# Kernel tuning notes

Hardware: AMD Instinct MI355X
Metric: run time of the kernel (lower is better)

The kernel has to match this reference:

```python
import jax, jax.numpy as jnp
import numpy as np

HIDDEN = 1024
SEQ = 32768


def setup_inputs() -> dict:
    key = jax.random.key(0)
    k1, k2, k3, k4 = jax.random.split(key, 4)
    scale = 1.0 / np.sqrt(HIDDEN)
    return {
        "hidden": jax.random.normal(k1, (HIDDEN,), dtype=jnp.float32),
        "encoder_outputs": jax.random.normal(k2, (SEQ, HIDDEN), dtype=jnp.float32),
        "W": jax.random.normal(k3, (HIDDEN, HIDDEN), dtype=jnp.float32) * scale,
        "b": jax.random.normal(k4, (HIDDEN,), dtype=jnp.float32) * scale,
    }


def reference(hidden, encoder_outputs, W, b):
    # method == 'general': energy_i = Linear(enc_i); score_i = hidden . energy_i
    # Batched: energies = (enc @ W.T + b) @ hidden   -> [S]
    proj = jnp.einsum("sh,oh->so", encoder_outputs, W) + b  # [S, H]
    energies = proj @ hidden                                  # [S]
    attn = jax.nn.softmax(energies, axis=-1)                  # softmax over seq
    return attn[None, None, :]                                # [1, 1, S]
```

## Files before the change

### kernel.cpp

```cpp
#include <hip/hip_runtime.h>
#include <math.h>

#define H 1024
#define S 32768

__global__ void matvec_v_kernel(const float* __restrict__ W,
                                const float* __restrict__ hidden,
                                float* __restrict__ v) {
    __shared__ float sh[H];
    __shared__ float4 red[256];
    const int t = threadIdx.x;
    const int b = blockIdx.x;
    const int c = t & 7;
    const int j = t >> 3;

    *reinterpret_cast<float4*>(&sh[t * 4]) =
        *reinterpret_cast<const float4*>(&hidden[t * 4]);
    __syncthreads();

    const int colbase = b * 32 + c * 4;
    float4 acc = make_float4(0.f, 0.f, 0.f, 0.f);
#pragma unroll 8
    for (int k = 0; k < 32; ++k) {
        const int o = j + 32 * k;
        const float hv = sh[o];
        const float4 w = *reinterpret_cast<const float4*>(&W[(size_t)o * H + colbase]);
        acc.x += hv * w.x; acc.y += hv * w.y;
        acc.z += hv * w.z; acc.w += hv * w.w;
    }
    red[t] = acc;
    __syncthreads();
#pragma unroll
    for (int off = 128; off >= 8; off >>= 1) {
        if (t < off) {
            float4 a = red[t], bb = red[t + off];
            a.x += bb.x; a.y += bb.y; a.z += bb.z; a.w += bb.w;
            red[t] = a;
        }
        __syncthreads();
    }
    if (t < 8)
        *reinterpret_cast<float4*>(&v[b * 32 + t * 4]) = red[t];
}

__global__ void energies_kernel(const float* __restrict__ enc,
                                const float* __restrict__ v,
                                float* __restrict__ energies,
                                float* __restrict__ mpart,
                                float* __restrict__ spart) {
    const int wave = threadIdx.x >> 6;
    const int lane = threadIdx.x & 63;
    const int gwave = blockIdx.x * 4 + wave;
    const int s0 = gwave * 4;

    float4 vv[4];
#pragma unroll
    for (int j = 0; j < 4; ++j)
        vv[j] = *reinterpret_cast<const float4*>(&v[j * 256 + lane * 4]);

    float4 ev[4][4];
#pragma unroll
    for (int r = 0; r < 4; ++r) {
        const float* row = enc + (size_t)(s0 + r) * H;
#pragma unroll
        for (int j = 0; j < 4; ++j)
            ev[r][j] = *reinterpret_cast<const float4*>(&row[j * 256 + lane * 4]);
    }

    float e[4];
#pragma unroll
    for (int r = 0; r < 4; ++r) {
        float acc = ev[r][0].x * vv[0].x + ev[r][0].y * vv[0].y +
                    ev[r][0].z * vv[0].z + ev[r][0].w * vv[0].w;
#pragma unroll
        for (int j = 1; j < 4; ++j) {
            acc += ev[r][j].x * vv[j].x + ev[r][j].y * vv[j].y +
                   ev[r][j].z * vv[j].z + ev[r][j].w * vv[j].w;
        }
#pragma unroll
        for (int off = 32; off > 0; off >>= 1)
            acc += __shfl_xor(acc, off, 64);
        e[r] = acc;
    }

    if (lane == 0) {
        energies[s0 + 0] = e[0];
        energies[s0 + 1] = e[1];
        energies[s0 + 2] = e[2];
        energies[s0 + 3] = e[3];
    }

    const float mw = fmaxf(fmaxf(e[0], e[1]), fmaxf(e[2], e[3]));
    const float sw = __expf(e[0] - mw) + __expf(e[1] - mw) +
                     __expf(e[2] - mw) + __expf(e[3] - mw);

    __shared__ float lm[4], ls[4];
    if (lane == 0) { lm[wave] = mw; ls[wave] = sw; }
    __syncthreads();
    if (threadIdx.x == 0) {
        const float m = fmaxf(fmaxf(lm[0], lm[1]), fmaxf(lm[2], lm[3]));
        const float s = ls[0] * __expf(lm[0] - m) + ls[1] * __expf(lm[1] - m) +
                        ls[2] * __expf(lm[2] - m) + ls[3] * __expf(lm[3] - m);
        mpart[blockIdx.x] = m;
        spart[blockIdx.x] = s;
    }
}

__global__ void finalize_kernel(const float* __restrict__ energies,
                                const float* __restrict__ mpart,
                                const float* __restrict__ spart,
                                float* __restrict__ out) {
    const int t = threadIdx.x;
    const int lane = t & 63;
    const int wave = t >> 6;
    __shared__ float rm[4], rs[4];

    const float4 ma = *reinterpret_cast<const float4*>(&mpart[t * 8]);
    const float4 mb = *reinterpret_cast<const float4*>(&mpart[t * 8 + 4]);
    const float4 sa = *reinterpret_cast<const float4*>(&spart[t * 8]);
    const float4 sb = *reinterpret_cast<const float4*>(&spart[t * 8 + 4]);

    float mt = fmaxf(fmaxf(fmaxf(ma.x, ma.y), fmaxf(ma.z, ma.w)),
                     fmaxf(fmaxf(mb.x, mb.y), fmaxf(mb.z, mb.w)));
#pragma unroll
    for (int off = 32; off > 0; off >>= 1)
        mt = fmaxf(mt, __shfl_xor(mt, off, 64));
    if (lane == 0) rm[wave] = mt;
    __syncthreads();
    const float gm = fmaxf(fmaxf(rm[0], rm[1]), fmaxf(rm[2], rm[3]));

    float st = sa.x * __expf(ma.x - gm) + sa.y * __expf(ma.y - gm) +
               sa.z * __expf(ma.z - gm) + sa.w * __expf(ma.w - gm) +
               sb.x * __expf(mb.x - gm) + sb.y * __expf(mb.y - gm) +
               sb.z * __expf(mb.z - gm) + sb.w * __expf(mb.w - gm);
#pragma unroll
    for (int off = 32; off > 0; off >>= 1)
        st += __shfl_xor(st, off, 64);
    if (lane == 0) rs[wave] = st;
    __syncthreads();
    const float inv = 1.0f / (rs[0] + rs[1] + rs[2] + rs[3]);

    const int i = blockIdx.x * 256 + t;
    out[i] = __expf(energies[i] - gm) * inv;
}

extern "C" void kernel_launch(void* const* d_in, const int* in_sizes, int n_in,
                              void* d_out, int out_size, void* d_ws, size_t ws_size,
                              hipStream_t stream) {
    const float* hidden = (const float*)d_in[0];
    const float* enc    = (const float*)d_in[1];
    const float* W      = (const float*)d_in[2];
    float* out = (float*)d_out;

    float* v        = (float*)d_ws;
    float* energies = v + H;
    float* mpart    = energies + S;
    float* spart    = mpart + 2048;

    matvec_v_kernel<<<32, 256, 0, stream>>>(W, hidden, v);
    energies_kernel<<<2048, 256, 0, stream>>>(enc, v, energies, mpart, spart);
    finalize_kernel<<<128, 256, 0, stream>>>(energies, mpart, spart, out);
}
```

Baseline: 206.6 us.

## Split matvec across more blocks and map 16-lane groups per row in energies kernel

The W·hidden matvec now runs on 64 blocks of 16 columns each instead of 32 blocks of 32 columns, to spread the W read over more CUs. The energies kernel stages v in shared memory and gives each row to a 16-lane group that loads its row in two batches of 8 float4. This needs only a 4-step shuffle reduction per row and cuts register pressure from 16 float4 of encoder data to 8. The block still covers 16 rows, but memory access per lane is now strided in 256-byte chunks per row, which may change coalescing behaviour.

```diff
diff --git a/kernel.cpp b/kernel.cpp
--- a/kernel.cpp
+++ b/kernel.cpp
@@ -11,18 +11,18 @@
     __shared__ float4 red[256];
     const int t = threadIdx.x;
     const int b = blockIdx.x;
-    const int c = t & 7;
-    const int j = t >> 3;
+    const int c = t & 3;
+    const int j = t >> 2;
 
     *reinterpret_cast<float4*>(&sh[t * 4]) =
         *reinterpret_cast<const float4*>(&hidden[t * 4]);
     __syncthreads();
 
-    const int colbase = b * 32 + c * 4;
+    const int colbase = b * 16 + c * 4;
     float4 acc = make_float4(0.f, 0.f, 0.f, 0.f);
-#pragma unroll 8
-    for (int k = 0; k < 32; ++k) {
-        const int o = j + 32 * k;
+#pragma unroll
+    for (int k = 0; k < 16; ++k) {
+        const int o = j + 64 * k;
         const float hv = sh[o];
         const float4 w = *reinterpret_cast<const float4*>(&W[(size_t)o * H + colbase]);
         acc.x += hv * w.x; acc.y += hv * w.y;
@@ -31,7 +31,7 @@
     red[t] = acc;
     __syncthreads();
 #pragma unroll
-    for (int off = 128; off >= 8; off >>= 1) {
+    for (int off = 128; off >= 4; off >>= 1) {
         if (t < off) {
             float4 a = red[t], bb = red[t + off];
             a.x += bb.x; a.y += bb.y; a.z += bb.z; a.w += bb.w;
@@ -39,8 +39,8 @@
         }
         __syncthreads();
     }
-    if (t < 8)
-        *reinterpret_cast<float4*>(&v[b * 32 + t * 4]) = red[t];
+    if (t < 4)
+        *reinterpret_cast<float4*>(&v[b * 16 + t * 4]) = red[t];
 }
 
 __global__ void energies_kernel(const float* __restrict__ enc,
@@ -48,56 +48,56 @@
                                 float* __restrict__ energies,
                                 float* __restrict__ mpart,
                                 float* __restrict__ spart) {
-    const int wave = threadIdx.x >> 6;
-    const int lane = threadIdx.x & 63;
-    const int gwave = blockIdx.x * 4 + wave;
-    const int s0 = gwave * 4;
+    __shared__ float sv[H];
+    __shared__ float lm[4], ls[4];
+    const int t = threadIdx.x;
+    const int wave = t >> 6;
+    const int lane = t & 63;
+    const int grp  = lane >> 4;
+    const int gl   = lane & 15;
 
-    float4 vv[4];
+    *reinterpret_cast<float4*>(&sv[t * 4]) =
+        *reinterpret_cast<const float4*>(&v[t * 4]);
+
+    const int row = blockIdx.x * 16 + wave * 4 + grp;
+    const float* rp = enc + (size_t)row * H + gl * 4;
+    __syncthreads();
+
+    float4 ev[8];
+    float acc = 0.f;
+
 #pragma unroll
-    for (int j = 0; j < 4; ++j)
-        vv[j] = *reinterpret_cast<const float4*>(&v[j * 256 + lane * 4]);
-
-    float4 ev[4][4];
+    for (int s = 0; s < 8; ++s)
+        ev[s] = *reinterpret_cast<const float4*>(&rp[s * 64]);
 #pragma unroll
-    for (int r = 0; r < 4; ++r) {
-        const float* row = enc + (size_t)(s0 + r) * H;
+    for (int s = 0; s < 8; ++s) {
+        const float4 vv = *reinterpret_cast<const float4*>(&sv[s * 64 + gl * 4]);
+        acc += ev[s].x * vv.x + ev[s].y * vv.y + ev[s].z * vv.z + ev[s].w * vv.w;
+    }
 #pragma unroll
-        for (int j = 0; j < 4; ++j)
-            ev[r][j] = *reinterpret_cast<const float4*>(&row[j * 256 + lane * 4]);
+    for (int s = 0; s < 8; ++s)
+        ev[s] = *reinterpret_cast<const float4*>(&rp[(s + 8) * 64]);
+#pragma unroll
+    for (int s = 0; s < 8; ++s) {
+        const float4 vv = *reinterpret_cast<const float4*>(&sv[(s + 8) * 64 + gl * 4]);
+        acc += ev[s].x * vv.x + ev[s].y * vv.y + ev[s].z * vv.z + ev[s].w * vv.w;
     }
 
-    float e[4];
 #pragma unroll
-    for (int r = 0; r < 4; ++r) {
-        float acc = ev[r][0].x * vv[0].x + ev[r][0].y * vv[0].y +
-                    ev[r][0].z * vv[0].z + ev[r][0].w * vv[0].w;
-#pragma unroll
-        for (int j = 1; j < 4; ++j) {
-            acc += ev[r][j].x * vv[j].x + ev[r][j].y * vv[j].y +
-                   ev[r][j].z * vv[j].z + ev[r][j].w * vv[j].w;
-        }
-#pragma unroll
-        for (int off = 32; off > 0; off >>= 1)
-            acc += __shfl_xor(acc, off, 64);
-        e[r] = acc;
-    }
+    for (int off = 1; off <= 8; off <<= 1)
+        acc += __shfl_xor(acc, off, 64);
 
-    if (lane == 0) {
-        energies[s0 + 0] = e[0];
-        energies[s0 + 1] = e[1];
-        energies[s0 + 2] = e[2];
-        energies[s0 + 3] = e[3];
-    }
+    float mw = acc;
+    mw = fmaxf(mw, __shfl_xor(mw, 16, 64));
+    mw = fmaxf(mw, __shfl_xor(mw, 32, 64));
+    float sw = __expf(acc - mw);
+    sw += __shfl_xor(sw, 16, 64);
+    sw += __shfl_xor(sw, 32, 64);
 
-    const float mw = fmaxf(fmaxf(e[0], e[1]), fmaxf(e[2], e[3]));
-    const float sw = __expf(e[0] - mw) + __expf(e[1] - mw) +
-                     __expf(e[2] - mw) + __expf(e[3] - mw);
-
-    __shared__ float lm[4], ls[4];
+    if (gl == 0) energies[row] = acc;
     if (lane == 0) { lm[wave] = mw; ls[wave] = sw; }
     __syncthreads();
-    if (threadIdx.x == 0) {
+    if (t == 0) {
         const float m = fmaxf(fmaxf(lm[0], lm[1]), fmaxf(lm[2], lm[3]));
         const float s = ls[0] * __expf(lm[0] - m) + ls[1] * __expf(lm[1] - m) +
                         ls[2] * __expf(lm[2] - m) + ls[3] * __expf(lm[3] - m);
@@ -157,7 +157,7 @@
     float* mpart    = energies + S;
     float* spart    = mpart + 2048;
 
-    matvec_v_kernel<<<32, 256, 0, stream>>>(W, hidden, v);
+    matvec_v_kernel<<<64, 256, 0, stream>>>(W, hidden, v);
     energies_kernel<<<2048, 256, 0, stream>>>(enc, v, energies, mpart, spart);
     finalize_kernel<<<128, 256, 0, stream>>>(energies, mpart, spart, out);
 }
```

New measurement: 206.2 us. About the same (-0.2%).
